# Optimization experiments

Measured on AMD Instinct MI355X. Metric: run time of the kernel, lower is better.

Reference implementation:

```python
import jax, jax.numpy as jnp
import numpy as np

I, H, O = 8, 32, 1  # input_size, hidden_size, output_size


def setup_inputs() -> dict:
    key = jax.random.key(0)
    ks = jax.random.split(key, 7)
    B, T = 4096, 256
    s_ih = 1.0 / np.sqrt(H)
    inp = {
        "x": jax.random.normal(ks[0], (B, T, I), dtype=jnp.float32),
        # PyTorch nn.LSTM params, gate order [i, f, g, o]
        "W_ih": jax.random.uniform(ks[1], (4 * H, I), minval=-s_ih, maxval=s_ih, dtype=jnp.float32),
        "W_hh": jax.random.uniform(ks[2], (4 * H, H), minval=-s_ih, maxval=s_ih, dtype=jnp.float32),
        "b_ih": jax.random.uniform(ks[3], (4 * H,), minval=-s_ih, maxval=s_ih, dtype=jnp.float32),
        "b_hh": jax.random.uniform(ks[4], (4 * H,), minval=-s_ih, maxval=s_ih, dtype=jnp.float32),
        # nn.Linear(H, O)
        "W_out": jax.random.uniform(ks[5], (O, H), minval=-s_ih, maxval=s_ih, dtype=jnp.float32),
        "b_out": jax.random.uniform(ks[6], (O,), minval=-s_ih, maxval=s_ih, dtype=jnp.float32),
    }
    return inp


def _lstm_last_h(x, W_ih, W_hh, b_ih, b_hh):
    B = x.shape[0]
    # Precompute input projections for all steps: [T, B, 4H]
    x_proj = jnp.einsum("bti,gi->tbg", x, W_ih) + (b_ih + b_hh)
    h0 = jnp.zeros((B, H), dtype=x.dtype)
    c0 = jnp.zeros((B, H), dtype=x.dtype)

    def step(carry, xp):
        h, c = carry
        z = xp + h @ W_hh.T  # [B, 4H]
        i = jax.nn.sigmoid(z[:, 0 * H:1 * H])
        f = jax.nn.sigmoid(z[:, 1 * H:2 * H])
        g = jnp.tanh(z[:, 2 * H:3 * H])
        o = jax.nn.sigmoid(z[:, 3 * H:4 * H])
        c = f * c + i * g
        h = o * jnp.tanh(c)
        return (h, c), None

    (hT, _), _ = jax.lax.scan(step, (h0, c0), x_proj)
    return hT  # equals out[:, -1, :] for unidirectional batch_first LSTM


def reference(x, W_ih, W_hh, b_ih, b_hh, W_out, b_out):
    hT = _lstm_last_h(x, W_ih, W_hh, b_ih, b_hh)
    return hT @ W_out.T + b_out  # [B, O]
```

## Files before the change

### kernel.cpp

```cpp
#include <hip/hip_runtime.h>


#define T_LEN 256
#define LOG2E 1.4426950408889634f

typedef __attribute__((ext_vector_type(8))) short bf16x8;
typedef __attribute__((ext_vector_type(4))) float f32x4;

static __device__ inline short f2bf(float f) {
    union { float f; unsigned u; } v; v.f = f;
    unsigned u = v.u;
    unsigned r = (u + 0x7FFFu + ((u >> 16) & 1u)) >> 16;
    return (short)r;
}
static __device__ inline float bf2f(short s) {
    union { unsigned u; float f; } v;
    v.u = ((unsigned)(unsigned short)s) << 16;
    return v.f;
}

static __device__ inline float sig_p(float zp) {
    return __builtin_amdgcn_rcpf(1.f + __builtin_amdgcn_exp2f(-zp));
}
static __device__ inline float tanh_p(float zp) {
    return 2.f * __builtin_amdgcn_rcpf(1.f + __builtin_amdgcn_exp2f(-(zp + zp))) - 1.f;
}

__global__ __launch_bounds__(256) void lstm_kernel(
    const float* __restrict__ x, const float* __restrict__ W_ih,
    const float* __restrict__ W_hh, const float* __restrict__ b_ih,
    const float* __restrict__ b_hh, const float* __restrict__ W_out,
    const float* __restrict__ b_out, float* __restrict__ out)
{
    __shared__ __attribute__((aligned(16))) short h_lds[2][16 * 40];

    const int tid  = threadIdx.x;
    const int w    = tid >> 6;
    const int lane = tid & 63;
    const int L    = lane & 15;
    const int q    = lane >> 4;
    const int row0 = blockIdx.x * 16;

    bf16x8 whh[2], wih[2];
    f32x4  bias4[2];
#pragma unroll
    for (int p = 0; p < 2; ++p) {
        const int n = 32 * (L & 3) + 8 * w + 4 * p + (L >> 2);
        const float* src = W_hh + n * 32 + q * 8;
        bf16x8 fr;
#pragma unroll
        for (int j = 0; j < 8; ++j) fr[j] = f2bf(src[j] * LOG2E);
        whh[p] = fr;
        bf16x8 gr = (bf16x8){0,0,0,0,0,0,0,0};
        if (q == 0) {
            const float* s2 = W_ih + n * 8;
#pragma unroll
            for (int j = 0; j < 8; ++j) gr[j] = f2bf(s2[j] * LOG2E);
        }
        wih[p] = gr;
        f32x4 bb;
#pragma unroll
        for (int r = 0; r < 4; ++r) {
            const int nr = 32 * r + 8 * w + 4 * p + q;
            bb[r] = (b_ih[nr] + b_hh[nr]) * LOG2E;
        }
        bias4[p] = bb;
    }

    for (int i = tid; i < 16 * 40; i += 256) h_lds[0][i] = 0;

    const float4* xv = (const float4*)x;
    const size_t xbase = (size_t)(row0 + L) * (T_LEN * 8 / 4);
    float4 xr0[2] = {{0,0,0,0},{0,0,0,0}}, xr1[2] = {{0,0,0,0},{0,0,0,0}};
    if (q == 0) {
        xr0[0] = xv[xbase + 0]; xr1[0] = xv[xbase + 1];
        xr0[1] = xv[xbase + 2]; xr1[1] = xv[xbase + 3];
    }

    float c0 = 0.f, c1 = 0.f;
    const int jme = 8 * w + q;

    __syncthreads();

#pragma unroll 2
    for (int t = 0; t < T_LEN; ++t) {
        const int par = t & 1;
        bf16x8 hfrag = *(const bf16x8*)(&h_lds[par][L * 40 + q * 8]);

        bf16x8 xfrag = (bf16x8){0,0,0,0,0,0,0,0};
        if (q == 0) {
            const float4 a = xr0[par], b = xr1[par];
            xfrag[0] = f2bf(a.x); xfrag[1] = f2bf(a.y);
            xfrag[2] = f2bf(a.z); xfrag[3] = f2bf(a.w);
            xfrag[4] = f2bf(b.x); xfrag[5] = f2bf(b.y);
            xfrag[6] = f2bf(b.z); xfrag[7] = f2bf(b.w);
            int tn = t + 2; if (tn >= T_LEN) tn = T_LEN - 1;
            xr0[par] = xv[xbase + (size_t)tn * 2];
            xr1[par] = xv[xbase + (size_t)tn * 2 + 1];
        }

        f32x4 acc[2];
#pragma unroll
        for (int p = 0; p < 2; ++p) {
            f32x4 z = __builtin_amdgcn_mfma_f32_16x16x32_bf16(wih[p], xfrag, bias4[p], 0, 0, 0);
            z = __builtin_amdgcn_mfma_f32_16x16x32_bf16(whh[p], hfrag, z, 0, 0, 0);
            acc[p] = z;
        }

        {
            const float i0 = sig_p(acc[0][0]), f0 = sig_p(acc[0][1]);
            const float g0 = tanh_p(acc[0][2]), o0 = sig_p(acc[0][3]);
            const float i1 = sig_p(acc[1][0]), f1 = sig_p(acc[1][1]);
            const float g1 = tanh_p(acc[1][2]), o1 = sig_p(acc[1][3]);
            c0 = fmaf(f0, c0, i0 * g0);
            c1 = fmaf(f1, c1, i1 * g1);
            const float h0 = o0 * tanh_p(c0 * LOG2E);
            const float h1 = o1 * tanh_p(c1 * LOG2E);
            short* dst = &h_lds[par ^ 1][L * 40 + jme];
            dst[0] = f2bf(h0);
            dst[4] = f2bf(h1);
        }

        __builtin_amdgcn_fence(__ATOMIC_RELEASE, "workgroup", "local");
        __builtin_amdgcn_s_barrier();
        __builtin_amdgcn_fence(__ATOMIC_ACQUIRE, "workgroup", "local");
    }

    if (tid < 16) {
        float s = b_out[0];
#pragma unroll
        for (int k = 0; k < 32; ++k) s = fmaf(bf2f(h_lds[0][tid * 40 + k]), W_out[k], s);
        out[row0 + tid] = s;
    }
}

extern "C" void kernel_launch(void* const* d_in, const int* in_sizes, int n_in,
                              void* d_out, int out_size, void* d_ws, size_t ws_size,
                              hipStream_t stream) {
    const float* x     = (const float*)d_in[0];
    const float* W_ih  = (const float*)d_in[1];
    const float* W_hh  = (const float*)d_in[2];
    const float* b_ih  = (const float*)d_in[3];
    const float* b_hh  = (const float*)d_in[4];
    const float* W_out = (const float*)d_in[5];
    const float* b_out = (const float*)d_in[6];
    float* out = (float*)d_out;

    const int B = in_sizes[0] / (T_LEN * 8);
    const int tiles = B / 16;
    lstm_kernel<<<tiles, 256, 0, stream>>>(x, W_ih, W_hh, b_ih, b_hh, W_out, b_out, out);
}
```

Before: 165.7 us.

## Split gate work across 8 waves and precompute next-step input projection

Doubles the workgroup to 512 threads so each wave owns one 16-column gate slice instead of two. Per-wave MFMA and activation work per timestep is halved, shortening the serial critical path. The x-projection MFMA for step t+1 is issued right after the recurrent MFMA of step t, taking it off the dependency chain. The cost is more waves per barrier and more threads per workgroup, which can reduce how many workgroups fit per CU.

```diff
diff --git a/kernel.cpp b/kernel.cpp
--- a/kernel.cpp
+++ b/kernel.cpp
@@ -18,7 +18,6 @@
     v.u = ((unsigned)(unsigned short)s) << 16;
     return v.f;
 }
-
 static __device__ inline float sig_p(float zp) {
     return __builtin_amdgcn_rcpf(1.f + __builtin_amdgcn_exp2f(-zp));
 }
@@ -26,7 +25,7 @@
     return 2.f * __builtin_amdgcn_rcpf(1.f + __builtin_amdgcn_exp2f(-(zp + zp))) - 1.f;
 }
 
-__global__ __launch_bounds__(256) void lstm_kernel(
+__global__ __launch_bounds__(512) void lstm_kernel(
     const float* __restrict__ x, const float* __restrict__ W_ih,
     const float* __restrict__ W_hh, const float* __restrict__ b_ih,
     const float* __restrict__ b_hh, const float* __restrict__ W_out,
@@ -41,33 +40,26 @@
     const int q    = lane >> 4;
     const int row0 = blockIdx.x * 16;
 
-    bf16x8 whh[2], wih[2];
-    f32x4  bias4[2];
+    const int n = 32 * (L & 3) + 4 * w + (L >> 2);
+    bf16x8 whh_f, wih_f = (bf16x8){0,0,0,0,0,0,0,0};
+    {
+        const float* src = W_hh + n * 32 + q * 8;
 #pragma unroll
-    for (int p = 0; p < 2; ++p) {
-        const int n = 32 * (L & 3) + 8 * w + 4 * p + (L >> 2);
-        const float* src = W_hh + n * 32 + q * 8;
-        bf16x8 fr;
-#pragma unroll
-        for (int j = 0; j < 8; ++j) fr[j] = f2bf(src[j] * LOG2E);
-        whh[p] = fr;
-        bf16x8 gr = (bf16x8){0,0,0,0,0,0,0,0};
+        for (int j = 0; j < 8; ++j) whh_f[j] = f2bf(src[j] * LOG2E);
         if (q == 0) {
             const float* s2 = W_ih + n * 8;
 #pragma unroll
-            for (int j = 0; j < 8; ++j) gr[j] = f2bf(s2[j] * LOG2E);
+            for (int j = 0; j < 8; ++j) wih_f[j] = f2bf(s2[j] * LOG2E);
         }
-        wih[p] = gr;
-        f32x4 bb;
+    }
+    f32x4 bias4;
 #pragma unroll
-        for (int r = 0; r < 4; ++r) {
-            const int nr = 32 * r + 8 * w + 4 * p + q;
-            bb[r] = (b_ih[nr] + b_hh[nr]) * LOG2E;
-        }
-        bias4[p] = bb;
+    for (int r = 0; r < 4; ++r) {
+        const int nr = 32 * r + 4 * w + q;
+        bias4[r] = (b_ih[nr] + b_hh[nr]) * LOG2E;
     }
 
-    for (int i = tid; i < 16 * 40; i += 256) h_lds[0][i] = 0;
+    for (int i = tid; i < 16 * 40; i += 512) h_lds[0][i] = 0;
 
     const float4* xv = (const float4*)x;
     const size_t xbase = (size_t)(row0 + L) * (T_LEN * 8 / 4);
@@ -77,8 +69,20 @@
         xr0[1] = xv[xbase + 2]; xr1[1] = xv[xbase + 3];
     }
 
-    float c0 = 0.f, c1 = 0.f;
-    const int jme = 8 * w + q;
+    float c = 0.f;
+    const int jme = 4 * w + q;
+
+    f32x4 zx;
+    {
+        bf16x8 xf = (bf16x8){0,0,0,0,0,0,0,0};
+        if (q == 0) {
+            const float4 a = xr0[0], b = xr1[0];
+            xf[0] = f2bf(a.x); xf[1] = f2bf(a.y); xf[2] = f2bf(a.z); xf[3] = f2bf(a.w);
+            xf[4] = f2bf(b.x); xf[5] = f2bf(b.y); xf[6] = f2bf(b.z); xf[7] = f2bf(b.w);
+            xr0[0] = xv[xbase + 4]; xr1[0] = xv[xbase + 5];
+        }
+        zx = __builtin_amdgcn_mfma_f32_16x16x32_bf16(wih_f, xf, bias4, 0, 0, 0);
+    }
 
     __syncthreads();
 
@@ -87,38 +91,30 @@
         const int par = t & 1;
         bf16x8 hfrag = *(const bf16x8*)(&h_lds[par][L * 40 + q * 8]);
 
-        bf16x8 xfrag = (bf16x8){0,0,0,0,0,0,0,0};
-        if (q == 0) {
-            const float4 a = xr0[par], b = xr1[par];
-            xfrag[0] = f2bf(a.x); xfrag[1] = f2bf(a.y);
-            xfrag[2] = f2bf(a.z); xfrag[3] = f2bf(a.w);
-            xfrag[4] = f2bf(b.x); xfrag[5] = f2bf(b.y);
-            xfrag[6] = f2bf(b.z); xfrag[7] = f2bf(b.w);
-            int tn = t + 2; if (tn >= T_LEN) tn = T_LEN - 1;
-            xr0[par] = xv[xbase + (size_t)tn * 2];
-            xr1[par] = xv[xbase + (size_t)tn * 2 + 1];
-        }
+        const f32x4 acc = __builtin_amdgcn_mfma_f32_16x16x32_bf16(whh_f, hfrag, zx, 0, 0, 0);
 
-        f32x4 acc[2];
-#pragma unroll
-        for (int p = 0; p < 2; ++p) {
-            f32x4 z = __builtin_amdgcn_mfma_f32_16x16x32_bf16(wih[p], xfrag, bias4[p], 0, 0, 0);
-            z = __builtin_amdgcn_mfma_f32_16x16x32_bf16(whh[p], hfrag, z, 0, 0, 0);
-            acc[p] = z;
+        {
+            const int ns = (t + 1) & 1;
+            bf16x8 xf = (bf16x8){0,0,0,0,0,0,0,0};
+            if (q == 0) {
+                const float4 a = xr0[ns], b = xr1[ns];
+                xf[0] = f2bf(a.x); xf[1] = f2bf(a.y); xf[2] = f2bf(a.z); xf[3] = f2bf(a.w);
+                xf[4] = f2bf(b.x); xf[5] = f2bf(b.y); xf[6] = f2bf(b.z); xf[7] = f2bf(b.w);
+                int tn = t + 3; if (tn >= T_LEN) tn = T_LEN - 1;
+                xr0[ns] = xv[xbase + (size_t)tn * 2];
+                xr1[ns] = xv[xbase + (size_t)tn * 2 + 1];
+            }
+            zx = __builtin_amdgcn_mfma_f32_16x16x32_bf16(wih_f, xf, bias4, 0, 0, 0);
         }
 
         {
-            const float i0 = sig_p(acc[0][0]), f0 = sig_p(acc[0][1]);
-            const float g0 = tanh_p(acc[0][2]), o0 = sig_p(acc[0][3]);
-            const float i1 = sig_p(acc[1][0]), f1 = sig_p(acc[1][1]);
-            const float g1 = tanh_p(acc[1][2]), o1 = sig_p(acc[1][3]);
-            c0 = fmaf(f0, c0, i0 * g0);
-            c1 = fmaf(f1, c1, i1 * g1);
-            const float h0 = o0 * tanh_p(c0 * LOG2E);
-            const float h1 = o1 * tanh_p(c1 * LOG2E);
-            short* dst = &h_lds[par ^ 1][L * 40 + jme];
-            dst[0] = f2bf(h0);
-            dst[4] = f2bf(h1);
+            const float iv = sig_p(acc[0]);
+            const float fv = sig_p(acc[1]);
+            const float gv = tanh_p(acc[2]);
+            const float ov = sig_p(acc[3]);
+            c = fmaf(fv, c, iv * gv);
+            const float hv = ov * tanh_p(c * LOG2E);
+            h_lds[par ^ 1][L * 40 + jme] = f2bf(hv);
         }
 
         __builtin_amdgcn_fence(__ATOMIC_RELEASE, "workgroup", "local");
@@ -148,5 +144,5 @@
 
     const int B = in_sizes[0] / (T_LEN * 8);
     const int tiles = B / 16;
-    lstm_kernel<<<tiles, 256, 0, stream>>>(x, W_ih, W_hh, b_ih, b_hh, W_out, b_out, out);
+    lstm_kernel<<<tiles, 512, 0, stream>>>(x, W_ih, W_hh, b_ih, b_hh, W_out, b_out, out);
 }
```

Result: no change. 167.2 us (+0.9%).

## Precompute next-step input MFMA off critical path and streamline gate math

Applied to the files above, without the earlier changes.

Moves the input-projection MFMA for step t+1 to after the barrier so only the recurrent MFMA sits on the serial dependency chain, and keeps h in registers (loaded right after the barrier) instead of re-reading LDS at loop top. Reorders gate columns so each lane writes two adjacent h values as one packed 32-bit LDS store. Folds the tanh doubling into the weights and merges sigmoid/tanh reciprocals into shared rcp calls with clamped exp2. It also swaps RNE rounding for a cheaper round-half-up bf16 conversion for activations, which slightly changes numerics.

```diff
diff --git a/kernel.cpp b/kernel.cpp
--- a/kernel.cpp
+++ b/kernel.cpp
@@ -4,26 +4,26 @@
 #define T_LEN 256
 #define LOG2E 1.4426950408889634f
 
-typedef __attribute__((ext_vector_type(8))) short bf16x8;
-typedef __attribute__((ext_vector_type(4))) float f32x4;
+typedef short bf16x8 __attribute__((ext_vector_type(8)));
+typedef float f32x4 __attribute__((ext_vector_type(4)));
 
-static __device__ inline short f2bf(float f) {
+static __device__ inline short f2bf_rne(float f) {
     union { float f; unsigned u; } v; v.f = f;
     unsigned u = v.u;
-    unsigned r = (u + 0x7FFFu + ((u >> 16) & 1u)) >> 16;
-    return (short)r;
+    return (short)((u + 0x7FFFu + ((u >> 16) & 1u)) >> 16);
+}
+static __device__ inline short f2bf_fast(float f) {
+    union { float f; unsigned u; } v; v.f = f;
+    return (short)((v.u + 0x8000u) >> 16);
+}
+static __device__ inline unsigned pack_bf2(float a, float b) {
+    union { float f; unsigned u; } x, y; x.f = a; y.f = b;
+    return ((x.u + 0x8000u) >> 16) | ((y.u + 0x8000u) & 0xFFFF0000u);
 }
 static __device__ inline float bf2f(short s) {
     union { unsigned u; float f; } v;
     v.u = ((unsigned)(unsigned short)s) << 16;
     return v.f;
-}
-
-static __device__ inline float sig_p(float zp) {
-    return __builtin_amdgcn_rcpf(1.f + __builtin_amdgcn_exp2f(-zp));
-}
-static __device__ inline float tanh_p(float zp) {
-    return 2.f * __builtin_amdgcn_rcpf(1.f + __builtin_amdgcn_exp2f(-(zp + zp))) - 1.f;
 }
 
 __global__ __launch_bounds__(256) void lstm_kernel(
@@ -42,88 +42,108 @@
     const int row0 = blockIdx.x * 16;
 
     bf16x8 whh[2], wih[2];
-    f32x4  bias4[2];
+    f32x4  bias[2];
 #pragma unroll
-    for (int p = 0; p < 2; ++p) {
-        const int n = 32 * (L & 3) + 8 * w + 4 * p + (L >> 2);
+    for (int e = 0; e < 2; ++e) {
+        const int   n = 32 * (L & 3) + 8 * (L >> 2) + 2 * w + e;
+        const float s = ((L & 3) == 2 ? 2.f * LOG2E : LOG2E);
         const float* src = W_hh + n * 32 + q * 8;
         bf16x8 fr;
 #pragma unroll
-        for (int j = 0; j < 8; ++j) fr[j] = f2bf(src[j] * LOG2E);
-        whh[p] = fr;
+        for (int j = 0; j < 8; ++j) fr[j] = f2bf_rne(src[j] * s);
+        whh[e] = fr;
         bf16x8 gr = (bf16x8){0,0,0,0,0,0,0,0};
         if (q == 0) {
             const float* s2 = W_ih + n * 8;
 #pragma unroll
-            for (int j = 0; j < 8; ++j) gr[j] = f2bf(s2[j] * LOG2E);
+            for (int j = 0; j < 8; ++j) gr[j] = f2bf_rne(s2[j] * s);
         }
-        wih[p] = gr;
+        wih[e] = gr;
         f32x4 bb;
 #pragma unroll
         for (int r = 0; r < 4; ++r) {
-            const int nr = 32 * r + 8 * w + 4 * p + q;
-            bb[r] = (b_ih[nr] + b_hh[nr]) * LOG2E;
+            const int   nr = 32 * r + 8 * q + 2 * w + e;
+            const float sr = (r == 2 ? 2.f * LOG2E : LOG2E);
+            bb[r] = (b_ih[nr] + b_hh[nr]) * sr;
         }
-        bias4[p] = bb;
+        bias[e] = bb;
     }
 
-    for (int i = tid; i < 16 * 40; i += 256) h_lds[0][i] = 0;
-
     const float4* xv = (const float4*)x;
-    const size_t xbase = (size_t)(row0 + L) * (T_LEN * 8 / 4);
+    const size_t  xb = (size_t)(row0 + L) * (T_LEN * 8 / 4);
     float4 xr0[2] = {{0,0,0,0},{0,0,0,0}}, xr1[2] = {{0,0,0,0},{0,0,0,0}};
+    bf16x8 xf0 = (bf16x8){0,0,0,0,0,0,0,0};
     if (q == 0) {
-        xr0[0] = xv[xbase + 0]; xr1[0] = xv[xbase + 1];
-        xr0[1] = xv[xbase + 2]; xr1[1] = xv[xbase + 3];
+        const float4 a = xv[xb + 0], b = xv[xb + 1];
+        xf0[0] = f2bf_fast(a.x); xf0[1] = f2bf_fast(a.y);
+        xf0[2] = f2bf_fast(a.z); xf0[3] = f2bf_fast(a.w);
+        xf0[4] = f2bf_fast(b.x); xf0[5] = f2bf_fast(b.y);
+        xf0[6] = f2bf_fast(b.z); xf0[7] = f2bf_fast(b.w);
+        xr0[1] = xv[xb + 2]; xr1[1] = xv[xb + 3];
+        xr0[0] = xv[xb + 4]; xr1[0] = xv[xb + 5];
     }
 
+    f32x4 zx[2];
+    zx[0] = __builtin_amdgcn_mfma_f32_16x16x32_bf16(wih[0], xf0, bias[0], 0, 0, 0);
+    zx[1] = __builtin_amdgcn_mfma_f32_16x16x32_bf16(wih[1], xf0, bias[1], 0, 0, 0);
+
+    bf16x8 hfrag = (bf16x8){0,0,0,0,0,0,0,0};
     float c0 = 0.f, c1 = 0.f;
-    const int jme = 8 * w + q;
-
-    __syncthreads();
 
 #pragma unroll 2
     for (int t = 0; t < T_LEN; ++t) {
-        const int par = t & 1;
-        bf16x8 hfrag = *(const bf16x8*)(&h_lds[par][L * 40 + q * 8]);
+        const int nxt = (t + 1) & 1;
 
-        bf16x8 xfrag = (bf16x8){0,0,0,0,0,0,0,0};
-        if (q == 0) {
-            const float4 a = xr0[par], b = xr1[par];
-            xfrag[0] = f2bf(a.x); xfrag[1] = f2bf(a.y);
-            xfrag[2] = f2bf(a.z); xfrag[3] = f2bf(a.w);
-            xfrag[4] = f2bf(b.x); xfrag[5] = f2bf(b.y);
-            xfrag[6] = f2bf(b.z); xfrag[7] = f2bf(b.w);
-            int tn = t + 2; if (tn >= T_LEN) tn = T_LEN - 1;
-            xr0[par] = xv[xbase + (size_t)tn * 2];
-            xr1[par] = xv[xbase + (size_t)tn * 2 + 1];
+        const f32x4 a0 = __builtin_amdgcn_mfma_f32_16x16x32_bf16(whh[0], hfrag, zx[0], 0, 0, 0);
+        const f32x4 a1 = __builtin_amdgcn_mfma_f32_16x16x32_bf16(whh[1], hfrag, zx[1], 0, 0, 0);
+
+        float h0, h1;
+        {
+            const float ei = __builtin_amdgcn_exp2f(fminf(-a0[0], 40.f));
+            const float ef = __builtin_amdgcn_exp2f(fminf(-a0[1], 40.f));
+            const float eg = __builtin_amdgcn_exp2f(fminf(-a0[2], 40.f));
+            const float eo = __builtin_amdgcn_exp2f(fminf(-a0[3], 40.f));
+            const float fv = __builtin_amdgcn_rcpf(1.f + ef);
+            const float ig = (1.f - eg) * __builtin_amdgcn_rcpf((1.f + ei) * (1.f + eg));
+            c0 = fmaf(fv, c0, ig);
+            const float ec = __builtin_amdgcn_exp2f(fminf(c0 * (-2.f * LOG2E), 40.f));
+            h0 = (1.f - ec) * __builtin_amdgcn_rcpf((1.f + eo) * (1.f + ec));
+        }
+        {
+            const float ei = __builtin_amdgcn_exp2f(fminf(-a1[0], 40.f));
+            const float ef = __builtin_amdgcn_exp2f(fminf(-a1[1], 40.f));
+            const float eg = __builtin_amdgcn_exp2f(fminf(-a1[2], 40.f));
+            const float eo = __builtin_amdgcn_exp2f(fminf(-a1[3], 40.f));
+            const float fv = __builtin_amdgcn_rcpf(1.f + ef);
+            const float ig = (1.f - eg) * __builtin_amdgcn_rcpf((1.f + ei) * (1.f + eg));
+            c1 = fmaf(fv, c1, ig);
+            const float ec = __builtin_amdgcn_exp2f(fminf(c1 * (-2.f * LOG2E), 40.f));
+            h1 = (1.f - ec) * __builtin_amdgcn_rcpf((1.f + eo) * (1.f + ec));
         }
 
-        f32x4 acc[2];
-#pragma unroll
-        for (int p = 0; p < 2; ++p) {
-            f32x4 z = __builtin_amdgcn_mfma_f32_16x16x32_bf16(wih[p], xfrag, bias4[p], 0, 0, 0);
-            z = __builtin_amdgcn_mfma_f32_16x16x32_bf16(whh[p], hfrag, z, 0, 0, 0);
-            acc[p] = z;
-        }
-
-        {
-            const float i0 = sig_p(acc[0][0]), f0 = sig_p(acc[0][1]);
-            const float g0 = tanh_p(acc[0][2]), o0 = sig_p(acc[0][3]);
-            const float i1 = sig_p(acc[1][0]), f1 = sig_p(acc[1][1]);
-            const float g1 = tanh_p(acc[1][2]), o1 = sig_p(acc[1][3]);
-            c0 = fmaf(f0, c0, i0 * g0);
-            c1 = fmaf(f1, c1, i1 * g1);
-            const float h0 = o0 * tanh_p(c0 * LOG2E);
-            const float h1 = o1 * tanh_p(c1 * LOG2E);
-            short* dst = &h_lds[par ^ 1][L * 40 + jme];
-            dst[0] = f2bf(h0);
-            dst[4] = f2bf(h1);
-        }
+        *(unsigned*)(&h_lds[nxt][L * 40 + 8 * q + 2 * w]) = pack_bf2(h0, h1);
 
         __builtin_amdgcn_fence(__ATOMIC_RELEASE, "workgroup", "local");
         __builtin_amdgcn_s_barrier();
         __builtin_amdgcn_fence(__ATOMIC_ACQUIRE, "workgroup", "local");
+
+        hfrag = *(const bf16x8*)(&h_lds[nxt][L * 40 + q * 8]);
+
+        {
+            const float4 a = xr0[nxt], b = xr1[nxt];
+            bf16x8 xf;
+            xf[0] = f2bf_fast(a.x); xf[1] = f2bf_fast(a.y);
+            xf[2] = f2bf_fast(a.z); xf[3] = f2bf_fast(a.w);
+            xf[4] = f2bf_fast(b.x); xf[5] = f2bf_fast(b.y);
+            xf[6] = f2bf_fast(b.z); xf[7] = f2bf_fast(b.w);
+            zx[0] = __builtin_amdgcn_mfma_f32_16x16x32_bf16(wih[0], xf, bias[0], 0, 0, 0);
+            zx[1] = __builtin_amdgcn_mfma_f32_16x16x32_bf16(wih[1], xf, bias[1], 0, 0, 0);
+            if (q == 0) {
+                int tn = t + 3; if (tn >= T_LEN) tn = T_LEN - 1;
+                xr0[nxt] = xv[xb + (size_t)tn * 2];
+                xr1[nxt] = xv[xb + (size_t)tn * 2 + 1];
+            }
+        }
     }
 
     if (tid < 16) {
```

Result: no change. 163.4 us (-1.4%).
